# Kernel tuning notes

Measured on AMD Instinct MI355X. Metric: run time of the kernel, lower is better.

Reference implementation:

```python
import jax, jax.numpy as jnp
import numpy as np

N_NODES = 50000
N_EDGES = 20000
EDGE_SIZE = 32
IN_CH = 256
OUT_CH = 256


def setup_inputs() -> dict:
    key = jax.random.key(0)
    k1, k2, k3 = jax.random.split(key, 3)
    x = jax.random.normal(k1, (N_NODES, IN_CH), dtype=jnp.float32)
    hyperedges = jax.random.randint(k2, (N_EDGES, EDGE_SIZE), 0, N_NODES)
    weight = jax.random.normal(k3, (IN_CH, OUT_CH), dtype=jnp.float32)
    return {"x": x, "hyperedges": hyperedges, "weight": weight}


def reference(x, hyperedges, weight):
    # Gather node features per hyperedge and reduce ('sum' aggregation):
    # [E, K, C] -> [E, C]
    edge_sum = x[hyperedges].sum(axis=1)
    # Scatter-add each hyperedge's summed feature back to every member node.
    agg = jnp.zeros_like(x).at[hyperedges].add(edge_sum[:, None, :])
    # Dense projection + ReLU.
    return jax.nn.relu(agg @ weight)
```

## Files before the change

kernel.cpp:

```cpp
#include <hip/hip_runtime.h>
#include <hip/hip_bf16.h>
#include <hip/hip_fp16.h>

#define N_NODES 50000
#define N_EDGES 20000
#define EDGE_K  32
#define CH      256
#define N_INC   (N_EDGES * EDGE_K)
#define ELL_CAP 64
#define NSLICE  8
#define SCH     32
#define ZROW    N_EDGES

typedef __attribute__((ext_vector_type(4))) float f32x4;
typedef __attribute__((ext_vector_type(8))) _Float16 f16x8;

static __device__ __forceinline__ __half2 u2h2(unsigned int u) {
    __half2 h; __builtin_memcpy(&h, &u, 4); return h;
}
static __device__ __forceinline__ unsigned int h22u(__half2 h) {
    unsigned int u; __builtin_memcpy(&u, &h, 4); return u;
}
static __device__ __forceinline__ unsigned int pk2h(float a, float b) {
    return h22u(__halves2half2(__float2half_rn(a), __float2half_rn(b)));
}

#define CONV_BLOCKS (N_NODES * CH / 8 / 256)
#define ZERO_BLOCKS ((N_NODES + 255) / 256)
#define ELLI_BLOCKS (N_NODES * ELL_CAP / 2 / 256)
__global__ void prep_kernel(const float* __restrict__ x, unsigned short* __restrict__ xb,
                            const float* __restrict__ w, unsigned short* __restrict__ wt,
                            int* __restrict__ deg, unsigned int* __restrict__ ellu,
                            unsigned short* __restrict__ yb) {
    int b = blockIdx.x;
    if (b < CONV_BLOCKS) {
        int i = b * 256 + threadIdx.x;
        int n = i >> 5, sub = i & 31;
        int g = sub >> 2, cp = (sub & 3) * 8;
        const float* src = x + (size_t)n * CH + sub * 8;
        f32x4 v0 = *reinterpret_cast<const f32x4*>(src);
        f32x4 v1 = *reinterpret_cast<const f32x4*>(src + 4);
        uint4 u;
        u.x = pk2h(v0.x, v0.y);
        u.y = pk2h(v0.z, v0.w);
        u.z = pk2h(v1.x, v1.y);
        u.w = pk2h(v1.z, v1.w);
        *reinterpret_cast<uint4*>(xb + ((size_t)g * N_NODES + n) * SCH + cp) = u;
    } else if (b < CONV_BLOCKS + CH) {
        int n = b - CONV_BLOCKS;
        int k = threadIdx.x;
        __half h = __float2half_rn(w[k * CH + n]);
        wt[n * CH + k] = *reinterpret_cast<unsigned short*>(&h);
    } else if (b < CONV_BLOCKS + CH + ZERO_BLOCKS) {
        int i = (b - CONV_BLOCKS - CH) * 256 + threadIdx.x;
        if (i < N_NODES) deg[i] = 0;
    } else if (b < CONV_BLOCKS + CH + ZERO_BLOCKS + ELLI_BLOCKS) {
        int i = (b - CONV_BLOCKS - CH - ZERO_BLOCKS) * 256 + threadIdx.x;
        ellu[i] = 0x4E204E20u;
    } else {
        int g = threadIdx.x >> 5, c = threadIdx.x & 31;
        yb[((size_t)g * (N_EDGES + 1) + ZROW) * SCH + c] = 0;
    }
}

#define FILL_GROUPS   8
#define NODES_PER_GRP (N_NODES / FILL_GROUPS)
#define FILL_WIN      2560
#define FILL_BLOCKS   ((N_INC / FILL_WIN) * FILL_GROUPS)
#define GGRP          (N_EDGES / 16)
#define GATHER_BLOCKS (GGRP * NSLICE)
__global__ __launch_bounds__(256, 4) void gather_fill_kernel(
        const unsigned short* __restrict__ xb, const int* __restrict__ he,
        unsigned short* __restrict__ es, int* __restrict__ deg,
        unsigned short* __restrict__ ell) {
    int b = blockIdx.x;
    if (b < FILL_BLOCKS) {
        int g  = b % FILL_GROUPS;
        int wn = b / FILL_GROUPS;
        int lo = g * NODES_PER_GRP, hi = lo + NODES_PER_GRP;
        int base = wn * FILL_WIN;
#pragma unroll
        for (int it = 0; it < FILL_WIN / 256; ++it) {
            int i = base + it * 256 + threadIdx.x;
            int node = he[i];
            if (node >= lo && node < hi) {
                int slot = atomicAdd(&deg[node], 1);
                if (slot < ELL_CAP)
                    ell[(size_t)node * ELL_CAP + slot] = (unsigned short)(i >> 5);
            }
        }
        return;
    }
    int gb  = b - FILL_BLOCKS;
    int g   = gb & 7;
    int grp = gb >> 3;
    int w = threadIdx.x >> 6, lane = threadIdx.x & 63;
    int ebase = grp * 16 + w * 4;
    const int* hp = he + (size_t)ebase * EDGE_K;
    int s = lane & 15;
    int ep = lane >> 4, k = (lane >> 2) & 3, q = lane & 3;
    int mA = hp[ep * 32 + s];
    int mB = hp[ep * 32 + 16 + s];
    const unsigned short* xg = xb + (size_t)g * N_NODES * SCH;
    int hb = lane & 48;
    int e0 = __shfl(mA, hb + ((0 + k) & 15), 64);
    int e1 = __shfl(mA, hb + ((4 + k) & 15), 64);
    int e2 = __shfl(mA, hb + ((8 + k) & 15), 64);
    int e3 = __shfl(mA, hb + ((12 + k) & 15), 64);
    int e4 = __shfl(mB, hb + ((0 + k) & 15), 64);
    int e5 = __shfl(mB, hb + ((4 + k) & 15), 64);
    int e6 = __shfl(mB, hb + ((8 + k) & 15), 64);
    int e7 = __shfl(mB, hb + ((12 + k) & 15), 64);
    uint4 d0 = *reinterpret_cast<const uint4*>(xg + (size_t)e0 * SCH + q * 8);
    uint4 d1 = *reinterpret_cast<const uint4*>(xg + (size_t)e1 * SCH + q * 8);
    uint4 d2 = *reinterpret_cast<const uint4*>(xg + (size_t)e2 * SCH + q * 8);
    uint4 d3 = *reinterpret_cast<const uint4*>(xg + (size_t)e3 * SCH + q * 8);
    uint4 d4 = *reinterpret_cast<const uint4*>(xg + (size_t)e4 * SCH + q * 8);
    uint4 d5 = *reinterpret_cast<const uint4*>(xg + (size_t)e5 * SCH + q * 8);
    uint4 d6 = *reinterpret_cast<const uint4*>(xg + (size_t)e6 * SCH + q * 8);
    uint4 d7 = *reinterpret_cast<const uint4*>(xg + (size_t)e7 * SCH + q * 8);
    __half2 a0 = u2h2(0u), a1 = u2h2(0u), a2 = u2h2(0u), a3 = u2h2(0u);
    a0 = __hadd2(a0, u2h2(d0.x)); a1 = __hadd2(a1, u2h2(d0.y));
    a2 = __hadd2(a2, u2h2(d0.z)); a3 = __hadd2(a3, u2h2(d0.w));
    a0 = __hadd2(a0, u2h2(d1.x)); a1 = __hadd2(a1, u2h2(d1.y));
    a2 = __hadd2(a2, u2h2(d1.z)); a3 = __hadd2(a3, u2h2(d1.w));
    a0 = __hadd2(a0, u2h2(d2.x)); a1 = __hadd2(a1, u2h2(d2.y));
    a2 = __hadd2(a2, u2h2(d2.z)); a3 = __hadd2(a3, u2h2(d2.w));
    a0 = __hadd2(a0, u2h2(d3.x)); a1 = __hadd2(a1, u2h2(d3.y));
    a2 = __hadd2(a2, u2h2(d3.z)); a3 = __hadd2(a3, u2h2(d3.w));
    a0 = __hadd2(a0, u2h2(d4.x)); a1 = __hadd2(a1, u2h2(d4.y));
    a2 = __hadd2(a2, u2h2(d4.z)); a3 = __hadd2(a3, u2h2(d4.w));
    a0 = __hadd2(a0, u2h2(d5.x)); a1 = __hadd2(a1, u2h2(d5.y));
    a2 = __hadd2(a2, u2h2(d5.z)); a3 = __hadd2(a3, u2h2(d5.w));
    a0 = __hadd2(a0, u2h2(d6.x)); a1 = __hadd2(a1, u2h2(d6.y));
    a2 = __hadd2(a2, u2h2(d6.z)); a3 = __hadd2(a3, u2h2(d6.w));
    a0 = __hadd2(a0, u2h2(d7.x)); a1 = __hadd2(a1, u2h2(d7.y));
    a2 = __hadd2(a2, u2h2(d7.z)); a3 = __hadd2(a3, u2h2(d7.w));
    a0 = __hadd2(a0, u2h2(__shfl_xor(h22u(a0), 4, 64)));
    a1 = __hadd2(a1, u2h2(__shfl_xor(h22u(a1), 4, 64)));
    a2 = __hadd2(a2, u2h2(__shfl_xor(h22u(a2), 4, 64)));
    a3 = __hadd2(a3, u2h2(__shfl_xor(h22u(a3), 4, 64)));
    a0 = __hadd2(a0, u2h2(__shfl_xor(h22u(a0), 8, 64)));
    a1 = __hadd2(a1, u2h2(__shfl_xor(h22u(a1), 8, 64)));
    a2 = __hadd2(a2, u2h2(__shfl_xor(h22u(a2), 8, 64)));
    a3 = __hadd2(a3, u2h2(__shfl_xor(h22u(a3), 8, 64)));
    if ((lane & 12) == 0) {
        uint4 u;
        u.x = h22u(a0); u.y = h22u(a1); u.z = h22u(a2); u.w = h22u(a3);
        *reinterpret_cast<uint4*>(es + (size_t)(ebase + ep) * CH + g * SCH + q * 8) = u;
    }
}

__global__ __launch_bounds__(256) void gemm_kernel(const unsigned short* __restrict__ es,
                                                   const unsigned short* __restrict__ wt,
                                                   unsigned short* __restrict__ yb) {
    int wid  = threadIdx.x >> 6;
    int lane = threadIdx.x & 63;
    int m0   = blockIdx.x * 64 + wid * 16;
    if (m0 >= N_EDGES) return;
    int lr = lane & 15;
    int lg = lane >> 4;

    f32x4 acc[16] = {};
    const unsigned short* arow = es + (size_t)(m0 + lr) * CH + lg * 8;
#pragma unroll
    for (int kk = 0; kk < CH; kk += 32) {
        f16x8 a = *reinterpret_cast<const f16x8*>(arow + kk);
#pragma unroll
        for (int nt = 0; nt < 16; ++nt) {
            f16x8 bb = *reinterpret_cast<const f16x8*>(
                wt + (size_t)(nt * 16 + lr) * CH + kk + lg * 8);
            acc[nt] = __builtin_amdgcn_mfma_f32_16x16x32_f16(a, bb, acc[nt], 0, 0, 0);
        }
    }
#pragma unroll
    for (int nt = 0; nt < 16; ++nt) {
#pragma unroll
        for (int r = 0; r < 4; ++r) {
            int row = m0 + lg * 4 + r;
            __half h = __float2half_rn(acc[nt][r]);
            yb[((size_t)(nt >> 1) * (N_EDGES + 1) + row) * SCH + (nt & 1) * 16 + lr] =
                *reinterpret_cast<unsigned short*>(&h);
        }
    }
}

#define AP_NPB    16
#define AP_BLOCKS ((N_NODES / AP_NPB) * NSLICE)
__global__ __launch_bounds__(256) void apply_kernel(
        const unsigned short* __restrict__ yb, const int* __restrict__ deg,
        const unsigned short* __restrict__ ell, float* __restrict__ out) {
    int b = blockIdx.x;
    int g = b & 7;
    int w = threadIdx.x >> 6, lane = threadIdx.x & 63;
    int np = lane >> 4, s = lane & 15, k = (lane >> 2) & 3, q = lane & 3;
    int node = (b >> 3) * AP_NPB + w * 4 + np;
    int d = deg[node];
    if (d > ELL_CAP) d = ELL_CAP;
    const unsigned short* er = ell + (size_t)node * ELL_CAP;
    int m0 = er[s], m1 = er[16 + s], m2 = er[32 + s], m3 = er[48 + s];
    int dmax = d;
    dmax = max(dmax, __shfl_xor(dmax, 16, 64));
    dmax = max(dmax, __shfl_xor(dmax, 32, 64));
    const unsigned short* yg = yb + (size_t)g * (N_EDGES + 1) * SCH;
    int hb = lane & 48;
    __half2 a0 = u2h2(0u), a1 = u2h2(0u), a2 = u2h2(0u), a3 = u2h2(0u);
    for (int rq = 0; rq < 4; ++rq) {
        if (rq * 16 >= dmax) break;
        int m = (rq == 0) ? m0 : (rq == 1) ? m1 : (rq == 2) ? m2 : m3;
        int e0 = __shfl(m, hb + 0 + k, 64);
        int e1 = __shfl(m, hb + 4 + k, 64);
        int e2 = __shfl(m, hb + 8 + k, 64);
        int e3 = __shfl(m, hb + 12 + k, 64);
        uint4 d0 = *reinterpret_cast<const uint4*>(yg + (size_t)e0 * SCH + q * 8);
        uint4 d1 = *reinterpret_cast<const uint4*>(yg + (size_t)e1 * SCH + q * 8);
        uint4 d2 = *reinterpret_cast<const uint4*>(yg + (size_t)e2 * SCH + q * 8);
        uint4 d3 = *reinterpret_cast<const uint4*>(yg + (size_t)e3 * SCH + q * 8);
        a0 = __hadd2(a0, u2h2(d0.x)); a1 = __hadd2(a1, u2h2(d0.y));
        a2 = __hadd2(a2, u2h2(d0.z)); a3 = __hadd2(a3, u2h2(d0.w));
        a0 = __hadd2(a0, u2h2(d1.x)); a1 = __hadd2(a1, u2h2(d1.y));
        a2 = __hadd2(a2, u2h2(d1.z)); a3 = __hadd2(a3, u2h2(d1.w));
        a0 = __hadd2(a0, u2h2(d2.x)); a1 = __hadd2(a1, u2h2(d2.y));
        a2 = __hadd2(a2, u2h2(d2.z)); a3 = __hadd2(a3, u2h2(d2.w));
        a0 = __hadd2(a0, u2h2(d3.x)); a1 = __hadd2(a1, u2h2(d3.y));
        a2 = __hadd2(a2, u2h2(d3.z)); a3 = __hadd2(a3, u2h2(d3.w));
    }
    a0 = __hadd2(a0, u2h2(__shfl_xor(h22u(a0), 4, 64)));
    a1 = __hadd2(a1, u2h2(__shfl_xor(h22u(a1), 4, 64)));
    a2 = __hadd2(a2, u2h2(__shfl_xor(h22u(a2), 4, 64)));
    a3 = __hadd2(a3, u2h2(__shfl_xor(h22u(a3), 4, 64)));
    a0 = __hadd2(a0, u2h2(__shfl_xor(h22u(a0), 8, 64)));
    a1 = __hadd2(a1, u2h2(__shfl_xor(h22u(a1), 8, 64)));
    a2 = __hadd2(a2, u2h2(__shfl_xor(h22u(a2), 8, 64)));
    a3 = __hadd2(a3, u2h2(__shfl_xor(h22u(a3), 8, 64)));
    if ((lane & 12) == 0) {
        float2 f0 = __half22float2(a0);
        float2 f1 = __half22float2(a1);
        float2 f2 = __half22float2(a2);
        float2 f3 = __half22float2(a3);
        f32x4 r0, r1;
        r0.x = fmaxf(f0.x, 0.f); r0.y = fmaxf(f0.y, 0.f);
        r0.z = fmaxf(f1.x, 0.f); r0.w = fmaxf(f1.y, 0.f);
        r1.x = fmaxf(f2.x, 0.f); r1.y = fmaxf(f2.y, 0.f);
        r1.z = fmaxf(f3.x, 0.f); r1.w = fmaxf(f3.y, 0.f);
        float* dst = out + (size_t)node * CH + g * SCH + q * 8;
        *reinterpret_cast<f32x4*>(dst)     = r0;
        *reinterpret_cast<f32x4*>(dst + 4) = r1;
    }
}

extern "C" void kernel_launch(void* const* d_in, const int* in_sizes, int n_in,
                              void* d_out, int out_size, void* d_ws, size_t ws_size,
                              hipStream_t stream) {
    const float* x  = (const float*)d_in[0];
    const int*   he = (const int*)d_in[1];
    const float* w  = (const float*)d_in[2];
    float* out = (float*)d_out;

    char* ws = (char*)d_ws;
    unsigned short* wt  = (unsigned short*)ws;
    unsigned short* es  = (unsigned short*)(ws + 131072);
    unsigned short* yb  = (unsigned short*)(ws + 10371072);
    int* deg = (int*)(ws + 20611584);
    unsigned short* ell = (unsigned short*)(ws + 20811584);

    unsigned short* xb = (unsigned short*)d_out;

    prep_kernel<<<CONV_BLOCKS + CH + ZERO_BLOCKS + ELLI_BLOCKS + 1, 256, 0, stream>>>(
        x, xb, w, wt, deg, (unsigned int*)ell, yb);

    gather_fill_kernel<<<FILL_BLOCKS + GATHER_BLOCKS, 256, 0, stream>>>(xb, he, es, deg, ell);

    {
        int blocks = (N_EDGES + 63) / 64;
        gemm_kernel<<<blocks, 256, 0, stream>>>(es, wt, yb);
    }

    apply_kernel<<<AP_BLOCKS, 256, 0, stream>>>(yb, deg, ell, out);
}
```

Before: 140.9 us.

## Split ELL fill across gather and GEMM kernels, drop ELL init, one edge per wave

The ELL adjacency fill is split in half. One half runs alongside the gather kernel and the other alongside the GEMM kernel, so the fill atomics overlap with more work. The ELL sentinel initialization is removed and deg zeroing moves to hipMemsetAsync. The apply kernel now masks unused slots to the zero row by comparing against the degree. The gather and apply kernels are remapped to one edge or node per wave with 32-lane index loads and a wider shuffle reduction, which means more blocks and shorter per-thread work.

New measurement: 199.7 us. 41.7% more time.

```diff
diff --git a/kernel.cpp b/kernel.cpp
--- a/kernel.cpp
+++ b/kernel.cpp
@@ -26,11 +26,8 @@
 }
 
 #define CONV_BLOCKS (N_NODES * CH / 8 / 256)
-#define ZERO_BLOCKS ((N_NODES + 255) / 256)
-#define ELLI_BLOCKS (N_NODES * ELL_CAP / 2 / 256)
 __global__ void prep_kernel(const float* __restrict__ x, unsigned short* __restrict__ xb,
                             const float* __restrict__ w, unsigned short* __restrict__ wt,
-                            int* __restrict__ deg, unsigned int* __restrict__ ellu,
                             unsigned short* __restrict__ yb) {
     int b = blockIdx.x;
     if (b < CONV_BLOCKS) {
@@ -51,12 +48,6 @@
         int k = threadIdx.x;
         __half h = __float2half_rn(w[k * CH + n]);
         wt[n * CH + k] = *reinterpret_cast<unsigned short*>(&h);
-    } else if (b < CONV_BLOCKS + CH + ZERO_BLOCKS) {
-        int i = (b - CONV_BLOCKS - CH) * 256 + threadIdx.x;
-        if (i < N_NODES) deg[i] = 0;
-    } else if (b < CONV_BLOCKS + CH + ZERO_BLOCKS + ELLI_BLOCKS) {
-        int i = (b - CONV_BLOCKS - CH - ZERO_BLOCKS) * 256 + threadIdx.x;
-        ellu[i] = 0x4E204E20u;
     } else {
         int g = threadIdx.x >> 5, c = threadIdx.x & 31;
         yb[((size_t)g * (N_EDGES + 1) + ZROW) * SCH + c] = 0;
@@ -66,76 +57,50 @@
 #define FILL_GROUPS   8
 #define NODES_PER_GRP (N_NODES / FILL_GROUPS)
 #define FILL_WIN      2560
-#define FILL_BLOCKS   ((N_INC / FILL_WIN) * FILL_GROUPS)
-#define GGRP          (N_EDGES / 16)
-#define GATHER_BLOCKS (GGRP * NSLICE)
-__global__ __launch_bounds__(256, 4) void gather_fill_kernel(
+#define FILLA_BLOCKS  ((N_INC / 2 / FILL_WIN) * FILL_GROUPS)
+#define FILLB_BLOCKS  FILLA_BLOCKS
+static __device__ __forceinline__ void fill_body(const int* __restrict__ he,
+                                                 int* __restrict__ deg,
+                                                 unsigned short* __restrict__ ell,
+                                                 int fb, int base_off) {
+    int g  = fb & 7;
+    int wn = fb >> 3;
+    int lo = g * NODES_PER_GRP, hi = lo + NODES_PER_GRP;
+    int base = base_off + wn * FILL_WIN;
+#pragma unroll
+    for (int it = 0; it < FILL_WIN / 256; ++it) {
+        int i = base + it * 256 + threadIdx.x;
+        int node = he[i];
+        if (node >= lo && node < hi) {
+            int slot = atomicAdd(&deg[node], 1);
+            if (slot < ELL_CAP)
+                ell[(size_t)node * ELL_CAP + slot] = (unsigned short)(i >> 5);
+        }
+    }
+}
+
+#define GATHER_BLOCKS ((N_EDGES / 4) * NSLICE)
+__global__ __launch_bounds__(256) void gather_fill_kernel(
         const unsigned short* __restrict__ xb, const int* __restrict__ he,
         unsigned short* __restrict__ es, int* __restrict__ deg,
         unsigned short* __restrict__ ell) {
     int b = blockIdx.x;
-    if (b < FILL_BLOCKS) {
-        int g  = b % FILL_GROUPS;
-        int wn = b / FILL_GROUPS;
-        int lo = g * NODES_PER_GRP, hi = lo + NODES_PER_GRP;
-        int base = wn * FILL_WIN;
-#pragma unroll
-        for (int it = 0; it < FILL_WIN / 256; ++it) {
-            int i = base + it * 256 + threadIdx.x;
-            int node = he[i];
-            if (node >= lo && node < hi) {
-                int slot = atomicAdd(&deg[node], 1);
-                if (slot < ELL_CAP)
-                    ell[(size_t)node * ELL_CAP + slot] = (unsigned short)(i >> 5);
-            }
-        }
-        return;
-    }
-    int gb  = b - FILL_BLOCKS;
-    int g   = gb & 7;
-    int grp = gb >> 3;
+    if (b < FILLA_BLOCKS) { fill_body(he, deg, ell, b, 0); return; }
+    int gb = b - FILLA_BLOCKS;
+    int g  = gb & 7;
     int w = threadIdx.x >> 6, lane = threadIdx.x & 63;
-    int ebase = grp * 16 + w * 4;
-    const int* hp = he + (size_t)ebase * EDGE_K;
-    int s = lane & 15;
-    int ep = lane >> 4, k = (lane >> 2) & 3, q = lane & 3;
-    int mA = hp[ep * 32 + s];
-    int mB = hp[ep * 32 + 16 + s];
+    int e = (gb >> 3) * 4 + w;
+    int myidx = he[e * EDGE_K + (lane & 31)];
+    int r = lane >> 2, q = lane & 3;
     const unsigned short* xg = xb + (size_t)g * N_NODES * SCH;
-    int hb = lane & 48;
-    int e0 = __shfl(mA, hb + ((0 + k) & 15), 64);
-    int e1 = __shfl(mA, hb + ((4 + k) & 15), 64);
-    int e2 = __shfl(mA, hb + ((8 + k) & 15), 64);
-    int e3 = __shfl(mA, hb + ((12 + k) & 15), 64);
-    int e4 = __shfl(mB, hb + ((0 + k) & 15), 64);
-    int e5 = __shfl(mB, hb + ((4 + k) & 15), 64);
-    int e6 = __shfl(mB, hb + ((8 + k) & 15), 64);
-    int e7 = __shfl(mB, hb + ((12 + k) & 15), 64);
+    int e0 = __shfl(myidx, r, 64);
+    int e1 = __shfl(myidx, 16 + r, 64);
     uint4 d0 = *reinterpret_cast<const uint4*>(xg + (size_t)e0 * SCH + q * 8);
     uint4 d1 = *reinterpret_cast<const uint4*>(xg + (size_t)e1 * SCH + q * 8);
-    uint4 d2 = *reinterpret_cast<const uint4*>(xg + (size_t)e2 * SCH + q * 8);
-    uint4 d3 = *reinterpret_cast<const uint4*>(xg + (size_t)e3 * SCH + q * 8);
-    uint4 d4 = *reinterpret_cast<const uint4*>(xg + (size_t)e4 * SCH + q * 8);
-    uint4 d5 = *reinterpret_cast<const uint4*>(xg + (size_t)e5 * SCH + q * 8);
-    uint4 d6 = *reinterpret_cast<const uint4*>(xg + (size_t)e6 * SCH + q * 8);
-    uint4 d7 = *reinterpret_cast<const uint4*>(xg + (size_t)e7 * SCH + q * 8);
-    __half2 a0 = u2h2(0u), a1 = u2h2(0u), a2 = u2h2(0u), a3 = u2h2(0u);
-    a0 = __hadd2(a0, u2h2(d0.x)); a1 = __hadd2(a1, u2h2(d0.y));
-    a2 = __hadd2(a2, u2h2(d0.z)); a3 = __hadd2(a3, u2h2(d0.w));
-    a0 = __hadd2(a0, u2h2(d1.x)); a1 = __hadd2(a1, u2h2(d1.y));
-    a2 = __hadd2(a2, u2h2(d1.z)); a3 = __hadd2(a3, u2h2(d1.w));
-    a0 = __hadd2(a0, u2h2(d2.x)); a1 = __hadd2(a1, u2h2(d2.y));
-    a2 = __hadd2(a2, u2h2(d2.z)); a3 = __hadd2(a3, u2h2(d2.w));
-    a0 = __hadd2(a0, u2h2(d3.x)); a1 = __hadd2(a1, u2h2(d3.y));
-    a2 = __hadd2(a2, u2h2(d3.z)); a3 = __hadd2(a3, u2h2(d3.w));
-    a0 = __hadd2(a0, u2h2(d4.x)); a1 = __hadd2(a1, u2h2(d4.y));
-    a2 = __hadd2(a2, u2h2(d4.z)); a3 = __hadd2(a3, u2h2(d4.w));
-    a0 = __hadd2(a0, u2h2(d5.x)); a1 = __hadd2(a1, u2h2(d5.y));
-    a2 = __hadd2(a2, u2h2(d5.z)); a3 = __hadd2(a3, u2h2(d5.w));
-    a0 = __hadd2(a0, u2h2(d6.x)); a1 = __hadd2(a1, u2h2(d6.y));
-    a2 = __hadd2(a2, u2h2(d6.z)); a3 = __hadd2(a3, u2h2(d6.w));
-    a0 = __hadd2(a0, u2h2(d7.x)); a1 = __hadd2(a1, u2h2(d7.y));
-    a2 = __hadd2(a2, u2h2(d7.z)); a3 = __hadd2(a3, u2h2(d7.w));
+    __half2 a0 = __hadd2(u2h2(d0.x), u2h2(d1.x));
+    __half2 a1 = __hadd2(u2h2(d0.y), u2h2(d1.y));
+    __half2 a2 = __hadd2(u2h2(d0.z), u2h2(d1.z));
+    __half2 a3 = __hadd2(u2h2(d0.w), u2h2(d1.w));
     a0 = __hadd2(a0, u2h2(__shfl_xor(h22u(a0), 4, 64)));
     a1 = __hadd2(a1, u2h2(__shfl_xor(h22u(a1), 4, 64)));
     a2 = __hadd2(a2, u2h2(__shfl_xor(h22u(a2), 4, 64)));
@@ -144,19 +109,32 @@
     a1 = __hadd2(a1, u2h2(__shfl_xor(h22u(a1), 8, 64)));
     a2 = __hadd2(a2, u2h2(__shfl_xor(h22u(a2), 8, 64)));
     a3 = __hadd2(a3, u2h2(__shfl_xor(h22u(a3), 8, 64)));
-    if ((lane & 12) == 0) {
+    a0 = __hadd2(a0, u2h2(__shfl_xor(h22u(a0), 16, 64)));
+    a1 = __hadd2(a1, u2h2(__shfl_xor(h22u(a1), 16, 64)));
+    a2 = __hadd2(a2, u2h2(__shfl_xor(h22u(a2), 16, 64)));
+    a3 = __hadd2(a3, u2h2(__shfl_xor(h22u(a3), 16, 64)));
+    a0 = __hadd2(a0, u2h2(__shfl_xor(h22u(a0), 32, 64)));
+    a1 = __hadd2(a1, u2h2(__shfl_xor(h22u(a1), 32, 64)));
+    a2 = __hadd2(a2, u2h2(__shfl_xor(h22u(a2), 32, 64)));
+    a3 = __hadd2(a3, u2h2(__shfl_xor(h22u(a3), 32, 64)));
+    if (r == 0) {
         uint4 u;
         u.x = h22u(a0); u.y = h22u(a1); u.z = h22u(a2); u.w = h22u(a3);
-        *reinterpret_cast<uint4*>(es + (size_t)(ebase + ep) * CH + g * SCH + q * 8) = u;
-    }
-}
-
-__global__ __launch_bounds__(256) void gemm_kernel(const unsigned short* __restrict__ es,
-                                                   const unsigned short* __restrict__ wt,
-                                                   unsigned short* __restrict__ yb) {
+        *reinterpret_cast<uint4*>(es + (size_t)e * CH + g * SCH + q * 8) = u;
+    }
+}
+
+#define GEMM_BLOCKS ((N_EDGES + 63) / 64)
+__global__ __launch_bounds__(256) void gemm_fill_kernel(
+        const unsigned short* __restrict__ es, const unsigned short* __restrict__ wt,
+        unsigned short* __restrict__ yb, const int* __restrict__ he,
+        int* __restrict__ deg, unsigned short* __restrict__ ell) {
+    int b = blockIdx.x;
+    if (b < FILLB_BLOCKS) { fill_body(he, deg, ell, b, N_INC / 2); return; }
+    int bb = b - FILLB_BLOCKS;
     int wid  = threadIdx.x >> 6;
     int lane = threadIdx.x & 63;
-    int m0   = blockIdx.x * 64 + wid * 16;
+    int m0   = bb * 64 + wid * 16;
     if (m0 >= N_EDGES) return;
     int lr = lane & 15;
     int lg = lane >> 4;
@@ -168,9 +146,9 @@
         f16x8 a = *reinterpret_cast<const f16x8*>(arow + kk);
 #pragma unroll
         for (int nt = 0; nt < 16; ++nt) {
-            f16x8 bb = *reinterpret_cast<const f16x8*>(
+            f16x8 bb2 = *reinterpret_cast<const f16x8*>(
                 wt + (size_t)(nt * 16 + lr) * CH + kk + lg * 8);
-            acc[nt] = __builtin_amdgcn_mfma_f32_16x16x32_f16(a, bb, acc[nt], 0, 0, 0);
+            acc[nt] = __builtin_amdgcn_mfma_f32_16x16x32_f16(a, bb2, acc[nt], 0, 0, 0);
         }
     }
 #pragma unroll
@@ -185,41 +163,35 @@
     }
 }
 
-#define AP_NPB    16
-#define AP_BLOCKS ((N_NODES / AP_NPB) * NSLICE)
+#define AP_BLOCKS ((N_NODES / 4) * NSLICE)
 __global__ __launch_bounds__(256) void apply_kernel(
         const unsigned short* __restrict__ yb, const int* __restrict__ deg,
         const unsigned short* __restrict__ ell, float* __restrict__ out) {
     int b = blockIdx.x;
     int g = b & 7;
     int w = threadIdx.x >> 6, lane = threadIdx.x & 63;
-    int np = lane >> 4, s = lane & 15, k = (lane >> 2) & 3, q = lane & 3;
-    int node = (b >> 3) * AP_NPB + w * 4 + np;
+    int node = (b >> 3) * 4 + w;
     int d = deg[node];
     if (d > ELL_CAP) d = ELL_CAP;
     const unsigned short* er = ell + (size_t)node * ELL_CAP;
-    int m0 = er[s], m1 = er[16 + s], m2 = er[32 + s], m3 = er[48 + s];
-    int dmax = d;
-    dmax = max(dmax, __shfl_xor(dmax, 16, 64));
-    dmax = max(dmax, __shfl_xor(dmax, 32, 64));
+    int m01 = er[lane & 31];
+    int r = lane >> 2, q = lane & 3;
     const unsigned short* yg = yb + (size_t)g * (N_EDGES + 1) * SCH;
-    int hb = lane & 48;
-    __half2 a0 = u2h2(0u), a1 = u2h2(0u), a2 = u2h2(0u), a3 = u2h2(0u);
-    for (int rq = 0; rq < 4; ++rq) {
-        if (rq * 16 >= dmax) break;
-        int m = (rq == 0) ? m0 : (rq == 1) ? m1 : (rq == 2) ? m2 : m3;
-        int e0 = __shfl(m, hb + 0 + k, 64);
-        int e1 = __shfl(m, hb + 4 + k, 64);
-        int e2 = __shfl(m, hb + 8 + k, 64);
-        int e3 = __shfl(m, hb + 12 + k, 64);
-        uint4 d0 = *reinterpret_cast<const uint4*>(yg + (size_t)e0 * SCH + q * 8);
+    int e0 = __shfl(m01, r, 64);      e0 = (r < d) ? e0 : ZROW;
+    uint4 d0 = *reinterpret_cast<const uint4*>(yg + (size_t)e0 * SCH + q * 8);
+    __half2 a0 = u2h2(d0.x), a1 = u2h2(d0.y), a2 = u2h2(d0.z), a3 = u2h2(d0.w);
+    if (d > 16) {
+        int e1 = __shfl(m01, 16 + r, 64); e1 = (16 + r < d) ? e1 : ZROW;
         uint4 d1 = *reinterpret_cast<const uint4*>(yg + (size_t)e1 * SCH + q * 8);
+        a0 = __hadd2(a0, u2h2(d1.x)); a1 = __hadd2(a1, u2h2(d1.y));
+        a2 = __hadd2(a2, u2h2(d1.z)); a3 = __hadd2(a3, u2h2(d1.w));
+    }
+    if (d > 32) {
+        int m23 = er[32 + (lane & 31)];
+        int e2 = __shfl(m23, r, 64);      e2 = (32 + r < d) ? e2 : ZROW;
+        int e3 = __shfl(m23, 16 + r, 64); e3 = (48 + r < d) ? e3 : ZROW;
         uint4 d2 = *reinterpret_cast<const uint4*>(yg + (size_t)e2 * SCH + q * 8);
         uint4 d3 = *reinterpret_cast<const uint4*>(yg + (size_t)e3 * SCH + q * 8);
-        a0 = __hadd2(a0, u2h2(d0.x)); a1 = __hadd2(a1, u2h2(d0.y));
-        a2 = __hadd2(a2, u2h2(d0.z)); a3 = __hadd2(a3, u2h2(d0.w));
-        a0 = __hadd2(a0, u2h2(d1.x)); a1 = __hadd2(a1, u2h2(d1.y));
-        a2 = __hadd2(a2, u2h2(d1.z)); a3 = __hadd2(a3, u2h2(d1.w));
         a0 = __hadd2(a0, u2h2(d2.x)); a1 = __hadd2(a1, u2h2(d2.y));
         a2 = __hadd2(a2, u2h2(d2.z)); a3 = __hadd2(a3, u2h2(d2.w));
         a0 = __hadd2(a0, u2h2(d3.x)); a1 = __hadd2(a1, u2h2(d3.y));
@@ -233,7 +205,15 @@
     a1 = __hadd2(a1, u2h2(__shfl_xor(h22u(a1), 8, 64)));
     a2 = __hadd2(a2, u2h2(__shfl_xor(h22u(a2), 8, 64)));
     a3 = __hadd2(a3, u2h2(__shfl_xor(h22u(a3), 8, 64)));
-    if ((lane & 12) == 0) {
+    a0 = __hadd2(a0, u2h2(__shfl_xor(h22u(a0), 16, 64)));
+    a1 = __hadd2(a1, u2h2(__shfl_xor(h22u(a1), 16, 64)));
+    a2 = __hadd2(a2, u2h2(__shfl_xor(h22u(a2), 16, 64)));
+    a3 = __hadd2(a3, u2h2(__shfl_xor(h22u(a3), 16, 64)));
+    a0 = __hadd2(a0, u2h2(__shfl_xor(h22u(a0), 32, 64)));
+    a1 = __hadd2(a1, u2h2(__shfl_xor(h22u(a1), 32, 64)));
+    a2 = __hadd2(a2, u2h2(__shfl_xor(h22u(a2), 32, 64)));
+    a3 = __hadd2(a3, u2h2(__shfl_xor(h22u(a3), 32, 64)));
+    if (r == 0) {
         float2 f0 = __half22float2(a0);
         float2 f1 = __half22float2(a1);
         float2 f2 = __half22float2(a2);
@@ -266,15 +246,15 @@
 
     unsigned short* xb = (unsigned short*)d_out;
 
-    prep_kernel<<<CONV_BLOCKS + CH + ZERO_BLOCKS + ELLI_BLOCKS + 1, 256, 0, stream>>>(
-        x, xb, w, wt, deg, (unsigned int*)ell, yb);
-
-    gather_fill_kernel<<<FILL_BLOCKS + GATHER_BLOCKS, 256, 0, stream>>>(xb, he, es, deg, ell);
-
-    {
-        int blocks = (N_EDGES + 63) / 64;
-        gemm_kernel<<<blocks, 256, 0, stream>>>(es, wt, yb);
-    }
+    hipMemsetAsync(deg, 0, (size_t)N_NODES * 4, stream);
+
+    prep_kernel<<<CONV_BLOCKS + CH + 1, 256, 0, stream>>>(x, xb, w, wt, yb);
+
+    gather_fill_kernel<<<FILLA_BLOCKS + GATHER_BLOCKS, 256, 0, stream>>>(
+        xb, he, es, deg, ell);
+
+    gemm_fill_kernel<<<FILLB_BLOCKS + GEMM_BLOCKS, 256, 0, stream>>>(
+        es, wt, yb, he, deg, ell);
 
     apply_kernel<<<AP_BLOCKS, 256, 0, stream>>>(yb, deg, ell, out);
 }
```
